# Kernel optimization log

Measured on AMD Instinct MI355X. Metric: run time of the kernel, lower is better.

Reference implementation:

```python
import jax, jax.numpy as jnp
import numpy as np

HID, H, HKV, D, INT, S, T = 2048, 16, 8, 128, 6144, 4096, 512
POS = 0          # absolute position of the first token in this prefill chunk
EPS = 1e-6
SCALE = 1.0 / D ** 0.5
REP = H // HKV


def setup_inputs() -> dict:
    key = jax.random.key(0)
    ks = jax.random.split(key, 12)
    w = lambda k, sh: jax.random.normal(k, sh, dtype=jnp.float32) * 0.02

    hidden_conv = jax.random.normal(ks[0], (1, HID, 1, T), dtype=jnp.float32)

    # RoPE tables for absolute positions POS..POS+T-1, HF half-rotation layout
    inv_freq = 1.0 / (10000.0 ** (jnp.arange(0, D, 2, dtype=jnp.float32) / D))
    pos = (POS + jnp.arange(T, dtype=jnp.float32))
    ang = pos[:, None] * inv_freq[None, :]                      # (T, D/2)
    emb = jnp.concatenate([ang, ang], axis=-1)                  # (T, D)
    cos = jnp.cos(emb)[None]                                    # (1, T, D)
    sin = jnp.sin(emb)[None]

    # one-hot write mask: column t has a 1 at row POS+t
    update_mask = jnp.zeros((S, T), jnp.float32).at[POS + jnp.arange(T), jnp.arange(T)].set(1.0)[None, None]
    # causal mask over the cache: slot s visible to token t iff s <= POS+t
    attn_mask = jnp.where(jnp.arange(S)[None, :] <= (POS + jnp.arange(T))[:, None], 0.0, -1e4).astype(jnp.float32)[None, None]

    k_cache = jnp.zeros((1, HKV, S, D), jnp.float32)
    v_cache = jnp.zeros((1, HKV, S, D), jnp.float32)

    return dict(
        hidden_conv=hidden_conv, cos=cos, sin=sin,
        update_mask=update_mask, attn_mask=attn_mask,
        k_cache=k_cache, v_cache=v_cache,
        wq=w(ks[1], (H * D, HID)), wk=w(ks[2], (HKV * D, HID)),
        wv=w(ks[3], (HKV * D, HID)), wo=w(ks[4], (HID, H * D)),
        ln1_w=jnp.ones((HID,), jnp.float32), ln2_w=jnp.ones((HID,), jnp.float32),
        qn_w=jnp.ones((D,), jnp.float32), kn_w=jnp.ones((D,), jnp.float32),
        w_gate_up=w(ks[5], (2 * INT, HID)), w_down=w(ks[6], (HID, INT)),
    )


def _rms(x, w):
    return x * jax.lax.rsqrt(jnp.mean(x * x, axis=-1, keepdims=True) + EPS) * w


def _rotate_half(x):
    x1, x2 = jnp.split(x, 2, axis=-1)
    return jnp.concatenate([-x2, x1], axis=-1)


def reference(hidden_conv, cos, sin, update_mask, attn_mask, k_cache, v_cache,
              wq, wk, wv, wo, ln1_w, ln2_w, qn_w, kn_w, w_gate_up, w_down):
    # (1, HID, 1, T) conv layout -> (1, T, HID)
    x = jnp.transpose(hidden_conv[:, :, 0, :], (0, 2, 1))

    h = _rms(x, ln1_w)
    # 1x1 conv == linear; channel order h*D+d matches view(1,H,D,T)
    q = jnp.einsum('btc,oc->bto', h, wq).reshape(1, T, H, D).transpose(0, 2, 1, 3)    # (1,H,T,D)
    k = jnp.einsum('btc,oc->bto', h, wk).reshape(1, T, HKV, D).transpose(0, 2, 1, 3)  # (1,HKV,T,D)
    v = jnp.einsum('btc,oc->bto', h, wv).reshape(1, T, HKV, D).transpose(0, 2, 1, 3)

    q = _rms(q, qn_w)
    k = _rms(k, kn_w)

    cos_b = cos[:, None]  # (1,1,T,D)
    sin_b = sin[:, None]
    q = q * cos_b + _rotate_half(q) * sin_b
    k = k * cos_b + _rotate_half(k) * sin_b

    # matmul-based KV cache write via one-hot mask (faithful to original)
    k_inc = jnp.matmul(update_mask, k)                 # (1,HKV,S,D)
    v_inc = jnp.matmul(update_mask, v)
    write_any = jnp.sum(update_mask, axis=-1, keepdims=True)  # (1,1,S,1)
    k_full = k_cache * (1.0 - write_any) + k_inc
    v_full = v_cache * (1.0 - write_any) + v_inc

    k_rep = jnp.repeat(k_full, REP, axis=1)            # (1,H,S,D)
    v_rep = jnp.repeat(v_full, REP, axis=1)

    scores = jnp.einsum('bhtd,bhsd->bhts', q, k_rep) * SCALE + attn_mask  # (1,H,T,S)
    attn = jax.nn.softmax(scores, axis=-1)
    out = jnp.einsum('bhts,bhsd->bhtd', attn, v_rep)   # (1,H,T,D)

    o_in = out.transpose(0, 2, 1, 3).reshape(1, T, H * D)
    attn_out = jnp.einsum('btc,oc->bto', o_in, wo)
    hidden = x + attn_out

    h2 = _rms(hidden, ln2_w)
    gate_up = jnp.einsum('btc,oc->bto', h2, w_gate_up)
    gate, up = jnp.split(gate_up, 2, axis=-1)
    mlp = jnp.einsum('bti,oi->bto', jax.nn.silu(gate) * up, w_down)
    hidden = hidden + mlp

    hidden_out = jnp.transpose(hidden, (0, 2, 1))[:, :, None, :]  # back to (1,HID,1,T)
    return hidden_out, k_full, v_full


if __name__ == '__main__':
    outs = reference(**setup_inputs())
    print([o.shape for o in outs])
```

## Files before the change

### kernel.cpp

```cpp
#include <hip/hip_runtime.h>
#include <hip/hip_bf16.h>
#include <hip/hip_fp16.h>

#define TT 512
#define HIDD 2048
#define NH 16
#define NKV 8
#define DD 128
#define INTR 6144
#define SEQ 4096
#define SCALE 0.08838834764831845f

typedef __attribute__((ext_vector_type(8))) short short8;
typedef __attribute__((ext_vector_type(4))) float floatx4;

static __device__ __forceinline__ unsigned short f2b(float f) {
  unsigned int u = __float_as_uint(f);
  u += 0x7fffu + ((u >> 16) & 1u);
  return (unsigned short)(u >> 16);
}

static __device__ __forceinline__ unsigned int f2b2(float a, float b) {
  __hip_bfloat162 h = __float22bfloat162_rn(make_float2(a, b));
  return *reinterpret_cast<unsigned int*>(&h);
}


static __device__ __forceinline__ void gld16(const void* g, void* l) {
  __builtin_amdgcn_global_load_lds(
      (const __attribute__((address_space(1))) unsigned int*)g,
      (__attribute__((address_space(3))) unsigned int*)l, 16, 0, 0);
}

template <int BM, bool B16>
static __device__ __forceinline__ void stage_tile(const unsigned short* __restrict__ A, int lda,
                                                  const void* __restrict__ B, int ldb, int k0,
                                                  unsigned char* buf, int wave, int lane) {
  {
    const int rpw = BM >> 2;
    const int rl = lane >> 2;
    const int c8 = (lane & 3) << 3;
#pragma unroll
    for (int i = 0; i < BM / 64; ++i) {
      const int rbase = wave * rpw + i * 16;
      gld16(A + (size_t)(rbase + rl) * lda + k0 + c8, buf + (size_t)rbase * 64);
    }
  }
  unsigned char* Bb = buf + BM * 64;
  if constexpr (B16) {
    const unsigned short* Bh = (const unsigned short*)B;
    const int rl = lane >> 2;
    const int c8 = (lane & 3) << 3;
#pragma unroll
    for (int i = 0; i < 2; ++i) {
      const int rbase = wave * 32 + i * 16;
      gld16(Bh + (size_t)(rbase + rl) * ldb + k0 + c8, Bb + (size_t)rbase * 64);
    }
  } else {
    const float* Bf = (const float*)B;
    const int rl = lane >> 3;
    const int sp = lane & 7;
#pragma unroll
    for (int i = 0; i < 4; ++i) {
      const int rbase = wave * 32 + i * 8;
      const int r = rbase + rl;
      gld16(Bf + (size_t)r * ldb + k0 + ((sp ^ (r & 7)) << 2), Bb + (size_t)rbase * 128);
    }
  }
}

template <int BM, bool B16>
static __device__ __forceinline__ void frags_from(const unsigned char* buf, int wr, int wc,
                                                  int lrow, int koff,
                                                  short8 (&af)[BM / 32], short8 (&bfr)[4]) {
  const unsigned short* Ab = (const unsigned short*)buf;
#pragma unroll
  for (int mi = 0; mi < BM / 32; ++mi)
    af[mi] = *reinterpret_cast<const short8*>(Ab + (size_t)(wr + mi * 16 + lrow) * 32 + koff);
  if constexpr (B16) {
    const unsigned short* Bb = (const unsigned short*)(buf + BM * 64);
#pragma unroll
    for (int ni = 0; ni < 4; ++ni)
      bfr[ni] = *reinterpret_cast<const short8*>(Bb + (size_t)(wc + ni * 16 + lrow) * 32 + koff);
  } else {
    const float* Bf = (const float*)(buf + BM * 64);
    const int s0 = koff >> 2;
#pragma unroll
    for (int ni = 0; ni < 4; ++ni) {
      const int r = wc + ni * 16 + lrow;
      const float4 x = *reinterpret_cast<const float4*>(Bf + (size_t)r * 32 + ((s0 ^ (r & 7)) << 2));
      const float4 y = *reinterpret_cast<const float4*>(Bf + (size_t)r * 32 + (((s0 + 1) ^ (r & 7)) << 2));
      union { short8 s; unsigned int u[4]; } pk;
      pk.u[0] = f2b2(x.x, x.y); pk.u[1] = f2b2(x.z, x.w);
      pk.u[2] = f2b2(y.x, y.y); pk.u[3] = f2b2(y.z, y.w);
      bfr[ni] = pk.s;
    }
  }
}

template <int BM, bool B16>
static __device__ __forceinline__ void gemm_core(const unsigned short* __restrict__ A, int lda,
                                                 const void* __restrict__ B, int ldb,
                                                 int kbeg, int kend, floatx4 (&acc)[BM / 32][4],
                                                 unsigned char* Ls) {
  constexpr int MI = BM / 32;
  constexpr int TILE = BM * 64 + (B16 ? 8192 : 16384);
  constexpr int NB = (BM / 64) + (B16 ? 2 : 4);
  const int tid = threadIdx.x;
  const int lane = tid & 63, wave = tid >> 6;
  const int wr = (wave >> 1) * (BM >> 1);
  const int wc = (wave & 1) << 6;
  const int lrow = lane & 15;
  const int koff = (lane >> 4) << 3;
  const int NT = (kend - kbeg) >> 5;
  stage_tile<BM, B16>(A, lda, B, ldb, kbeg,      Ls,        wave, lane);
  stage_tile<BM, B16>(A, lda, B, ldb, kbeg + 32, Ls + TILE, wave, lane);
  int p = 0;
  for (int t = 0; t < NT - 1; ++t) {
    if constexpr (NB == 6)      asm volatile("s_waitcnt vmcnt(6)" ::: "memory");
    else if constexpr (NB == 3) asm volatile("s_waitcnt vmcnt(3)" ::: "memory");
    else if constexpr (NB == 4) asm volatile("s_waitcnt vmcnt(4)" ::: "memory");
    else                        asm volatile("s_waitcnt vmcnt(5)" ::: "memory");
    __builtin_amdgcn_sched_barrier(0);
    __builtin_amdgcn_s_barrier();
    short8 af[MI], bfr[4];
    frags_from<BM, B16>(Ls + p * TILE, wr, wc, lrow, koff, af, bfr);
    asm volatile("s_waitcnt lgkmcnt(0)" ::: "memory");
    __builtin_amdgcn_sched_barrier(0);
    __builtin_amdgcn_s_barrier();
    if (t + 2 < NT)
      stage_tile<BM, B16>(A, lda, B, ldb, kbeg + (t + 2) * 32, Ls + p * TILE, wave, lane);
#pragma unroll
    for (int mi = 0; mi < MI; ++mi)
#pragma unroll
      for (int ni = 0; ni < 4; ++ni)
        acc[mi][ni] = __builtin_amdgcn_mfma_f32_16x16x32_bf16(af[mi], bfr[ni], acc[mi][ni], 0, 0, 0);
    p ^= 1;
  }
  asm volatile("s_waitcnt vmcnt(0)" ::: "memory");
  __builtin_amdgcn_sched_barrier(0);
  __builtin_amdgcn_s_barrier();
  {
    short8 af[MI], bfr[4];
    frags_from<BM, B16>(Ls + p * TILE, wr, wc, lrow, koff, af, bfr);
#pragma unroll
    for (int mi = 0; mi < MI; ++mi)
#pragma unroll
      for (int ni = 0; ni < 4; ++ni)
        acc[mi][ni] = __builtin_amdgcn_mfma_f32_16x16x32_bf16(af[mi], bfr[ni], acc[mi][ni], 0, 0, 0);
  }
}

#define EPI_VARS \
  const int lane = threadIdx.x & 63; \
  const int wave = threadIdx.x >> 6; \
  const int wc = (wave & 1) << 6;    \
  const int lrow = lane & 15;        \
  const int quad = lane >> 4;

#define ZERO_ACC(MI_) \
  floatx4 acc[MI_][4]; \
  _Pragma("unroll") for (int mi = 0; mi < MI_; ++mi) \
  _Pragma("unroll") for (int ni = 0; ni < 4; ++ni) { floatx4 z = {0.f, 0.f, 0.f, 0.f}; acc[mi][ni] = z; }

template <int S>
static __device__ __forceinline__ void swz(int b, int& mt, int& nt, int& s) {
  mt = (b >> 3) & 3;
  const int gid = ((b >> 5) << 3) | (b & 7);
  nt = gid / S;
  s = gid - nt * S;
}


__global__ __launch_bounds__(1024) void k_rms1(const float* __restrict__ conv,
                                               const float* __restrict__ w,
                                               float* __restrict__ xb,
                                               unsigned short* __restrict__ h1b) {
  const int t0 = blockIdx.x << 5;
  const int tid = threadIdx.x;
  const int j = tid & 31;
  const int g = tid >> 5;
  __shared__ float part[32][32];
  __shared__ float tile[32][33];
  __shared__ float rs[32];
  float ss = 0.f;
  for (int c0 = 0; c0 < HIDD; c0 += 32) {
    const float v = conv[(size_t)(c0 + g) * TT + t0 + j];
    ss += v * v;
  }
  part[g][j] = ss;
  __syncthreads();
  if (g == 0) {
    float tot = 0.f;
#pragma unroll
    for (int q = 0; q < 32; ++q) tot += part[q][j];
    rs[j] = rsqrtf(tot * (1.0f / HIDD) + 1e-6f);
  }
  __syncthreads();
  for (int c0 = 0; c0 < HIDD; c0 += 32) {
    tile[g][j] = conv[(size_t)(c0 + g) * TT + t0 + j];
    __syncthreads();
    const float v = tile[j][g];
    const float rv = rs[g];
    xb[(size_t)(t0 + g) * HIDD + c0 + j] = v;
    h1b[(size_t)(t0 + g) * HIDD + c0 + j] = f2b(v * rv * w[c0 + j]);
    __syncthreads();
  }
}

__global__ __launch_bounds__(256) void k_gemm_qkv(const unsigned short* __restrict__ h1b,
                                                  const float* __restrict__ wq,
                                                  const float* __restrict__ wk,
                                                  const float* __restrict__ wv,
                                                  float* __restrict__ Pq) {
  __shared__ __align__(16) unsigned char Ls[2 * (128 * 64 + 16384)];
  int mt, nt, s;
  swz<4>(blockIdx.x, mt, nt, s);
  const int m0 = mt << 7, n0 = nt << 7;
  const float* Bp;
  if (n0 < 2048)      Bp = wq + (size_t)n0 * HIDD;
  else if (n0 < 3072) Bp = wk + (size_t)(n0 - 2048) * HIDD;
  else                Bp = wv + (size_t)(n0 - 3072) * HIDD;
  ZERO_ACC(4)
  gemm_core<128, false>(h1b + (size_t)m0 * HIDD, HIDD, Bp, HIDD, s * 512, s * 512 + 512, acc, Ls);
  EPI_VARS
  const int wr = (wave >> 1) << 6;
  float* out = Pq + (size_t)s * (TT * 4096);
#pragma unroll
  for (int mi = 0; mi < 4; ++mi)
#pragma unroll
    for (int ni = 0; ni < 4; ++ni)
#pragma unroll
      for (int rr = 0; rr < 4; ++rr) {
        const int row = m0 + wr + mi * 16 + quad * 4 + rr;
        const int col = n0 + wc + ni * 16 + lrow;
        out[(size_t)row * 4096 + col] = acc[mi][ni][rr];
      }
}

__global__ __launch_bounds__(128) void k_rope(const float* __restrict__ Pq,
                                              const float* __restrict__ cosb,
                                              const float* __restrict__ sinb,
                                              const float* __restrict__ qnw,
                                              const float* __restrict__ knw,
                                              unsigned short* __restrict__ qb,
                                              unsigned short* __restrict__ kb,
                                              unsigned short* __restrict__ vtb,
                                              float* __restrict__ kout,
                                              float* __restrict__ vout) {
  const int u = blockIdx.x;
  const int t = blockIdx.y;
  const int d = threadIdx.x;
  __shared__ float red[2];
  __shared__ float sh[DD];
  int slot;
  if (u < NH)            slot = u * DD + d;
  else if (u < NH + NKV) slot = 2048 + (u - NH) * DD + d;
  else                   slot = 3072 + (u - NH - NKV) * DD + d;
  const size_t idx = (size_t)t * 4096 + slot;
  float val = Pq[idx] + Pq[idx + TT * 4096] + Pq[idx + 2 * TT * 4096] + Pq[idx + 3 * TT * 4096];
  if (u < NH + NKV) {
    float ss = val * val;
    const int lane = d & 63, wid = d >> 6;
#pragma unroll
    for (int o = 32; o; o >>= 1) ss += __shfl_xor(ss, o);
    if (!lane) red[wid] = ss;
    __syncthreads();
    const float r = rsqrtf((red[0] + red[1]) * (1.0f / DD) + 1e-6f);
    const float w = (u < NH) ? qnw[d] : knw[d];
    const float nv = val * r * w;
    sh[d] = nv;
    __syncthreads();
    const float partner = sh[d ^ 64];
    const float rh = (d < 64) ? -partner : partner;
    const float o = nv * cosb[(size_t)t * DD + d] + rh * sinb[(size_t)t * DD + d];
    if (u < NH) {
      qb[(size_t)u * TT * DD + (size_t)t * DD + d] = f2b(o);
    } else {
      const int kh = u - NH;
      kout[(size_t)kh * SEQ * DD + (size_t)t * DD + d] = o;
      kb[(size_t)kh * TT * DD + (size_t)t * DD + d] = f2b(o);
    }
  } else {
    const int vh = u - NH - NKV;
    vout[(size_t)vh * SEQ * DD + (size_t)t * DD + d] = val;
    vtb[(size_t)vh * DD * TT + (size_t)d * TT + t] = f2b(val);
  }
}

__global__ __launch_bounds__(256) void k_tail(const float* __restrict__ kc,
                                              const float* __restrict__ vc,
                                              float* __restrict__ ko,
                                              float* __restrict__ vo) {
  const int i = blockIdx.x * 256 + threadIdx.x;
  const int e = i << 2;
  const int s = (e >> 7) & (SEQ - 1);
  if (s >= TT) {
    reinterpret_cast<float4*>(ko)[i] = reinterpret_cast<const float4*>(kc)[i];
    reinterpret_cast<float4*>(vo)[i] = reinterpret_cast<const float4*>(vc)[i];
  }
}

__global__ __launch_bounds__(256) void k_scores(const unsigned short* __restrict__ qb,
                                                const unsigned short* __restrict__ kb,
                                                float* __restrict__ sc) {
  __shared__ __align__(16) unsigned char Ls[2 * (64 * 64 + 8192)];
  const int m0 = blockIdx.x << 6, n0 = blockIdx.y << 7, h = blockIdx.z;
  ZERO_ACC(2)
  gemm_core<64, true>(qb + (size_t)h * TT * DD + (size_t)m0 * DD, DD,
                      kb + (size_t)(h >> 1) * TT * DD + (size_t)n0 * DD, DD, 0, DD, acc, Ls);
  EPI_VARS
  const int wr = (wave >> 1) << 5;
  float* out = sc + (size_t)h * TT * TT;
#pragma unroll
  for (int mi = 0; mi < 2; ++mi)
#pragma unroll
    for (int ni = 0; ni < 4; ++ni)
#pragma unroll
      for (int rr = 0; rr < 4; ++rr) {
        const int t = m0 + wr + mi * 16 + quad * 4 + rr;
        const int s = n0 + wc + ni * 16 + lrow;
        float v = acc[mi][ni][rr] * SCALE;
        if (s > t) v += -10000.0f;
        out[(size_t)t * TT + s] = v;
      }
}

__global__ __launch_bounds__(256) void k_softmax(const float* __restrict__ sc,
                                                 unsigned short* __restrict__ Pb) {
  const int h = blockIdx.x >> 9, t = blockIdx.x & 511;
  const int tid = threadIdx.x;
  const float* row = sc + ((size_t)h * TT + t) * TT;
  float v0 = row[tid], v1 = row[tid + 256];
  __shared__ float red[4];
  const int lane = tid & 63, wid = tid >> 6;
  float m = fmaxf(v0, v1);
#pragma unroll
  for (int o = 32; o; o >>= 1) m = fmaxf(m, __shfl_xor(m, o));
  if (!lane) red[wid] = m;
  __syncthreads();
  m = fmaxf(fmaxf(red[0], red[1]), fmaxf(red[2], red[3]));
  const float e0 = __expf(v0 - m), e1 = __expf(v1 - m);
  float s = e0 + e1;
  __syncthreads();
#pragma unroll
  for (int o = 32; o; o >>= 1) s += __shfl_xor(s, o);
  if (!lane) red[wid] = s;
  __syncthreads();
  const float inv = 1.0f / (red[0] + red[1] + red[2] + red[3]);
  unsigned short* orow = Pb + ((size_t)h * TT + t) * TT;
  orow[tid] = f2b(e0 * inv);
  orow[tid + 256] = f2b(e1 * inv);
}

__global__ __launch_bounds__(256) void k_pv(const unsigned short* __restrict__ Pb,
                                            const unsigned short* __restrict__ vtb,
                                            float* __restrict__ Ppv) {
  __shared__ __align__(16) unsigned char Ls[2 * (64 * 64 + 8192)];
  const int m0 = blockIdx.x << 6, h = blockIdx.y, s = blockIdx.z;
  ZERO_ACC(2)
  gemm_core<64, true>(Pb + (size_t)h * TT * TT + (size_t)m0 * TT, TT,
                      vtb + (size_t)(h >> 1) * DD * TT, TT, s * 128, s * 128 + 128, acc, Ls);
  EPI_VARS
  const int wr = (wave >> 1) << 5;
  float* out = Ppv + (size_t)s * (TT * HIDD);
#pragma unroll
  for (int mi = 0; mi < 2; ++mi)
#pragma unroll
    for (int ni = 0; ni < 4; ++ni)
#pragma unroll
      for (int rr = 0; rr < 4; ++rr) {
        const int row = m0 + wr + mi * 16 + quad * 4 + rr;
        const int col = wc + ni * 16 + lrow;
        out[(size_t)row * HIDD + h * DD + col] = acc[mi][ni][rr];
      }
}

__global__ __launch_bounds__(256) void k_red_pv(const float* __restrict__ Ppv,
                                                unsigned short* __restrict__ o_inb) {
  const int i = blockIdx.x * 256 + threadIdx.x;
  const float4* p = reinterpret_cast<const float4*>(Ppv);
  float4 a = p[i];
  const float4 b = p[i + 262144], c = p[i + 524288], d = p[i + 786432];
  a.x += b.x + c.x + d.x; a.y += b.y + c.y + d.y;
  a.z += b.z + c.z + d.z; a.w += b.w + c.w + d.w;
  uint2 o;
  o.x = f2b2(a.x, a.y);
  o.y = f2b2(a.z, a.w);
  *reinterpret_cast<uint2*>(o_inb + (size_t)i * 4) = o;
}

__global__ __launch_bounds__(256) void k_gemm_o(const unsigned short* __restrict__ o_inb,
                                                const float* __restrict__ wo,
                                                float* __restrict__ Po) {
  __shared__ __align__(16) unsigned char Ls[2 * (128 * 64 + 16384)];
  int mt, nt, s;
  swz<8>(blockIdx.x, mt, nt, s);
  const int m0 = mt << 7, n0 = nt << 7;
  ZERO_ACC(4)
  gemm_core<128, false>(o_inb + (size_t)m0 * HIDD, HIDD, wo + (size_t)n0 * HIDD, HIDD,
                        s * 256, s * 256 + 256, acc, Ls);
  EPI_VARS
  const int wr = (wave >> 1) << 6;
  float* out = Po + (size_t)s * (TT * HIDD);
#pragma unroll
  for (int mi = 0; mi < 4; ++mi)
#pragma unroll
    for (int ni = 0; ni < 4; ++ni)
#pragma unroll
      for (int rr = 0; rr < 4; ++rr) {
        const int row = m0 + wr + mi * 16 + quad * 4 + rr;
        const int col = n0 + wc + ni * 16 + lrow;
        out[(size_t)row * HIDD + col] = acc[mi][ni][rr];
      }
}

__global__ __launch_bounds__(256) void k_rms2(const float* __restrict__ xb,
                                              const float* __restrict__ Po,
                                              const float* __restrict__ w,
                                              float* __restrict__ hidden,
                                              unsigned short* __restrict__ h2b) {
  const int t = blockIdx.x;
  const int tid = threadIdx.x;
  float2 v[4];
  float ss = 0.f;
#pragma unroll
  for (int i = 0; i < 4; ++i) {
    const int c = (tid << 1) + (i << 9);
    const size_t idx = (size_t)t * HIDD + c;
    float2 a = *reinterpret_cast<const float2*>(xb + idx);
#pragma unroll
    for (int sp = 0; sp < 8; ++sp) {
      const float2 b = *reinterpret_cast<const float2*>(Po + idx + (size_t)sp * (TT * HIDD));
      a.x += b.x; a.y += b.y;
    }
    v[i] = a;
    ss += a.x * a.x + a.y * a.y;
  }
  __shared__ float red[4];
  const int lane = tid & 63, wid = tid >> 6;
#pragma unroll
  for (int o = 32; o; o >>= 1) ss += __shfl_xor(ss, o);
  if (!lane) red[wid] = ss;
  __syncthreads();
  const float tot = red[0] + red[1] + red[2] + red[3];
  const float r = rsqrtf(tot * (1.0f / HIDD) + 1e-6f);
#pragma unroll
  for (int i = 0; i < 4; ++i) {
    const int c = (tid << 1) + (i << 9);
    const size_t idx = (size_t)t * HIDD + c;
    *reinterpret_cast<float2*>(hidden + idx) = v[i];
    const float2 wv2 = *reinterpret_cast<const float2*>(w + c);
    *reinterpret_cast<unsigned int*>(h2b + idx) = f2b2(v[i].x * r * wv2.x, v[i].y * r * wv2.y);
  }
}

__global__ __launch_bounds__(256) void k_gemm_gu(const unsigned short* __restrict__ h2b,
                                                 const float* __restrict__ wgu,
                                                 __half* __restrict__ guh) {
  __shared__ __align__(16) unsigned char Ls[2 * (128 * 64 + 16384)];
  int mt, nt, s;
  swz<2>(blockIdx.x, mt, nt, s);
  const int m0 = mt << 7, n0 = nt << 7;
  ZERO_ACC(4)
  gemm_core<128, false>(h2b + (size_t)m0 * HIDD, HIDD, wgu + (size_t)n0 * HIDD, HIDD,
                        s * 1024, s * 1024 + 1024, acc, Ls);
  EPI_VARS
  const int wr = (wave >> 1) << 6;
  __half* out = guh + (size_t)s * (TT * 2 * INTR);
#pragma unroll
  for (int mi = 0; mi < 4; ++mi)
#pragma unroll
    for (int ni = 0; ni < 4; ++ni)
#pragma unroll
      for (int rr = 0; rr < 4; ++rr) {
        const int row = m0 + wr + mi * 16 + quad * 4 + rr;
        const int col = n0 + wc + ni * 16 + lrow;
        out[(size_t)row * (2 * INTR) + col] = __float2half(acc[mi][ni][rr]);
      }
}

__global__ __launch_bounds__(256) void k_silu(const __half* __restrict__ guh,
                                              unsigned short* __restrict__ actb) {
  const int j0 = (blockIdx.x * 256 + threadIdx.x) << 1;
  const int t = blockIdx.y;
  const size_t base = (size_t)t * (2 * INTR) + j0;
  const size_t off = (size_t)TT * (2 * INTR);
  const float2 g0 = __half22float2(*reinterpret_cast<const __half2*>(guh + base));
  const float2 g1 = __half22float2(*reinterpret_cast<const __half2*>(guh + off + base));
  const float2 u0 = __half22float2(*reinterpret_cast<const __half2*>(guh + base + INTR));
  const float2 u1 = __half22float2(*reinterpret_cast<const __half2*>(guh + off + base + INTR));
  const float gx = g0.x + g1.x, gy = g0.y + g1.y;
  const float ux = u0.x + u1.x, uy = u0.y + u1.y;
  const float a0 = gx / (1.f + __expf(-gx)) * ux;
  const float a1 = gy / (1.f + __expf(-gy)) * uy;
  *reinterpret_cast<unsigned int*>(actb + (size_t)t * INTR + j0) = f2b2(a0, a1);
}

__global__ __launch_bounds__(256) void k_gemm_down(const unsigned short* __restrict__ actb,
                                                   const float* __restrict__ wdn,
                                                   float* __restrict__ Pdn) {
  __shared__ __align__(16) unsigned char Ls[2 * (128 * 64 + 16384)];
  int mt, nt, s;
  swz<8>(blockIdx.x, mt, nt, s);
  const int m0 = mt << 7, n0 = nt << 7;
  ZERO_ACC(4)
  gemm_core<128, false>(actb + (size_t)m0 * INTR, INTR, wdn + (size_t)n0 * INTR, INTR,
                        s * 768, s * 768 + 768, acc, Ls);
  EPI_VARS
  const int wr = (wave >> 1) << 6;
  float* out = Pdn + (size_t)s * (TT * HIDD);
#pragma unroll
  for (int mi = 0; mi < 4; ++mi)
#pragma unroll
    for (int ni = 0; ni < 4; ++ni)
#pragma unroll
      for (int rr = 0; rr < 4; ++rr) {
        const int row = m0 + wr + mi * 16 + quad * 4 + rr;
        const int col = n0 + wc + ni * 16 + lrow;
        out[(size_t)row * HIDD + col] = acc[mi][ni][rr];
      }
}

__global__ __launch_bounds__(256) void k_final(const float* __restrict__ hidden,
                                               const float* __restrict__ Pdn,
                                               float* __restrict__ out0) {
  __shared__ float tile[32][33];
  const int c0 = blockIdx.x << 5, t0 = blockIdx.y << 5;
  const int tx = threadIdx.x & 31, ty0 = (threadIdx.x >> 5) << 2;
#pragma unroll
  for (int i = 0; i < 4; ++i) {
    const int t = t0 + ty0 + i;
    const size_t idx = (size_t)t * HIDD + c0 + tx;
    float a = hidden[idx];
#pragma unroll
    for (int sp = 0; sp < 8; ++sp) a += Pdn[idx + (size_t)sp * (TT * HIDD)];
    tile[ty0 + i][tx] = a;
  }
  __syncthreads();
#pragma unroll
  for (int i = 0; i < 4; ++i)
    out0[(size_t)(c0 + ty0 + i) * TT + t0 + tx] = tile[tx][ty0 + i];
}

extern "C" void kernel_launch(void* const* d_in, const int* in_sizes, int n_in,
                              void* d_out, int out_size, void* d_ws, size_t ws_size,
                              hipStream_t stream) {
  const float* conv   = (const float*)d_in[0];
  const float* cosb   = (const float*)d_in[1];
  const float* sinb   = (const float*)d_in[2];
  const float* kcache = (const float*)d_in[5];
  const float* vcache = (const float*)d_in[6];
  const float* wq  = (const float*)d_in[7];
  const float* wk  = (const float*)d_in[8];
  const float* wv  = (const float*)d_in[9];
  const float* wo  = (const float*)d_in[10];
  const float* ln1 = (const float*)d_in[11];
  const float* ln2 = (const float*)d_in[12];
  const float* qnw = (const float*)d_in[13];
  const float* knw = (const float*)d_in[14];
  const float* wgu = (const float*)d_in[15];
  const float* wdn = (const float*)d_in[16];

  float* ws = (float*)d_ws;
  float* xb = ws + 0;
  unsigned short* h1b  = (unsigned short*)(ws + 1048576);
  unsigned short* o_inb = h1b;
  unsigned short* h2b  = (unsigned short*)(ws + 1572864);
  float* hidden = ws + 2097152;
  unsigned short* qb  = (unsigned short*)(ws + 3145728);
  unsigned short* kb  = qb + 1048576;
  unsigned short* vtb = kb + 524288;
  unsigned short* actb = (unsigned short*)(ws + 4194304);
  float* R   = ws + 5767168;
  float* Pq  = R;
  unsigned short* Pb = (unsigned short*)R;
  float* sc  = R + 2097152;
  float* Ppv = R + 2097152;
  float* Po  = R;
  __half* guh = (__half*)R;
  float* Pdn = R;

  float* out0 = (float*)d_out;
  float* kout = out0 + 1048576;
  float* vout = kout + 4194304;

  k_rms1<<<16, 1024, 0, stream>>>(conv, ln1, xb, h1b);
  k_gemm_qkv<<<512, 256, 0, stream>>>(h1b, wq, wk, wv, Pq);
  k_rope<<<dim3(NH + 2 * NKV, TT), 128, 0, stream>>>(Pq, cosb, sinb, qnw, knw, qb, kb, vtb, kout, vout);
  k_tail<<<4096, 256, 0, stream>>>(kcache, vcache, kout, vout);
  k_scores<<<dim3(8, 4, NH), 256, 0, stream>>>(qb, kb, sc);
  k_softmax<<<NH * TT, 256, 0, stream>>>(sc, Pb);
  k_pv<<<dim3(8, NH, 4), 256, 0, stream>>>(Pb, vtb, Ppv);
  k_red_pv<<<1024, 256, 0, stream>>>(Ppv, o_inb);
  k_gemm_o<<<512, 256, 0, stream>>>(o_inb, wo, Po);
  k_rms2<<<TT, 256, 0, stream>>>(xb, Po, ln2, hidden, h2b);
  k_gemm_gu<<<768, 256, 0, stream>>>(h2b, wgu, guh);
  k_silu<<<dim3(12, TT), 256, 0, stream>>>(guh, actb);
  k_gemm_down<<<512, 256, 0, stream>>>(actb, wdn, Pdn);
  k_final<<<dim3(HIDD / 32, TT / 32), 256, 0, stream>>>(hidden, Pdn, out0);
}
```

Measured before the change: 465.4 us.

## Use triple-buffered LDS ring in GEMM core to drop one barrier per k-step

Switches the shared GEMM main loop from a double buffer to a three-slot LDS ring. The next tile is now staged into a third slot while the current slot is read, so each iteration needs only one barrier instead of two plus an lgkmcnt wait. This trades 50% more LDS per block, which may reduce occupancy in the 128-row GEMMs (72 KB per block), for less synchronisation stall.

```diff
diff --git a/kernel.cpp b/kernel.cpp
--- a/kernel.cpp
+++ b/kernel.cpp
@@ -113,41 +113,31 @@
   const int lrow = lane & 15;
   const int koff = (lane >> 4) << 3;
   const int NT = (kend - kbeg) >> 5;
-  stage_tile<BM, B16>(A, lda, B, ldb, kbeg,      Ls,        wave, lane);
-  stage_tile<BM, B16>(A, lda, B, ldb, kbeg + 32, Ls + TILE, wave, lane);
-  int p = 0;
-  for (int t = 0; t < NT - 1; ++t) {
-    if constexpr (NB == 6)      asm volatile("s_waitcnt vmcnt(6)" ::: "memory");
-    else if constexpr (NB == 3) asm volatile("s_waitcnt vmcnt(3)" ::: "memory");
-    else if constexpr (NB == 4) asm volatile("s_waitcnt vmcnt(4)" ::: "memory");
-    else                        asm volatile("s_waitcnt vmcnt(5)" ::: "memory");
+  unsigned char* P0 = Ls;
+  unsigned char* P1 = Ls + TILE;
+  unsigned char* P2 = Ls + 2 * TILE;
+  stage_tile<BM, B16>(A, lda, B, ldb, kbeg,      P0, wave, lane);
+  stage_tile<BM, B16>(A, lda, B, ldb, kbeg + 32, P1, wave, lane);
+  for (int t = 0; t < NT; ++t) {
+    if (t + 1 < NT) {
+      if constexpr (NB == 6)      asm volatile("s_waitcnt vmcnt(6)" ::: "memory");
+      else if constexpr (NB == 4) asm volatile("s_waitcnt vmcnt(4)" ::: "memory");
+      else                        asm volatile("s_waitcnt vmcnt(3)" ::: "memory");
+    } else {
+      asm volatile("s_waitcnt vmcnt(0)" ::: "memory");
+    }
+    __builtin_amdgcn_s_barrier();
     __builtin_amdgcn_sched_barrier(0);
-    __builtin_amdgcn_s_barrier();
+    if (t + 2 < NT)
+      stage_tile<BM, B16>(A, lda, B, ldb, kbeg + (t + 2) * 32, P2, wave, lane);
     short8 af[MI], bfr[4];
-    frags_from<BM, B16>(Ls + p * TILE, wr, wc, lrow, koff, af, bfr);
-    asm volatile("s_waitcnt lgkmcnt(0)" ::: "memory");
-    __builtin_amdgcn_sched_barrier(0);
-    __builtin_amdgcn_s_barrier();
-    if (t + 2 < NT)
-      stage_tile<BM, B16>(A, lda, B, ldb, kbeg + (t + 2) * 32, Ls + p * TILE, wave, lane);
+    frags_from<BM, B16>(P0, wr, wc, lrow, koff, af, bfr);
 #pragma unroll
     for (int mi = 0; mi < MI; ++mi)
 #pragma unroll
       for (int ni = 0; ni < 4; ++ni)
         acc[mi][ni] = __builtin_amdgcn_mfma_f32_16x16x32_bf16(af[mi], bfr[ni], acc[mi][ni], 0, 0, 0);
-    p ^= 1;
-  }
-  asm volatile("s_waitcnt vmcnt(0)" ::: "memory");
-  __builtin_amdgcn_sched_barrier(0);
-  __builtin_amdgcn_s_barrier();
-  {
-    short8 af[MI], bfr[4];
-    frags_from<BM, B16>(Ls + p * TILE, wr, wc, lrow, koff, af, bfr);
-#pragma unroll
-    for (int mi = 0; mi < MI; ++mi)
-#pragma unroll
-      for (int ni = 0; ni < 4; ++ni)
-        acc[mi][ni] = __builtin_amdgcn_mfma_f32_16x16x32_bf16(af[mi], bfr[ni], acc[mi][ni], 0, 0, 0);
+    unsigned char* tmp = P0; P0 = P1; P1 = P2; P2 = tmp;
   }
 }
 
@@ -213,7 +203,7 @@
                                                   const float* __restrict__ wk,
                                                   const float* __restrict__ wv,
                                                   float* __restrict__ Pq) {
-  __shared__ __align__(16) unsigned char Ls[2 * (128 * 64 + 16384)];
+  __shared__ __align__(16) unsigned char Ls[3 * (128 * 64 + 16384)];
   int mt, nt, s;
   swz<4>(blockIdx.x, mt, nt, s);
   const int m0 = mt << 7, n0 = nt << 7;
@@ -304,7 +294,7 @@
 __global__ __launch_bounds__(256) void k_scores(const unsigned short* __restrict__ qb,
                                                 const unsigned short* __restrict__ kb,
                                                 float* __restrict__ sc) {
-  __shared__ __align__(16) unsigned char Ls[2 * (64 * 64 + 8192)];
+  __shared__ __align__(16) unsigned char Ls[3 * (64 * 64 + 8192)];
   const int m0 = blockIdx.x << 6, n0 = blockIdx.y << 7, h = blockIdx.z;
   ZERO_ACC(2)
   gemm_core<64, true>(qb + (size_t)h * TT * DD + (size_t)m0 * DD, DD,
@@ -356,7 +346,7 @@
 __global__ __launch_bounds__(256) void k_pv(const unsigned short* __restrict__ Pb,
                                             const unsigned short* __restrict__ vtb,
                                             float* __restrict__ Ppv) {
-  __shared__ __align__(16) unsigned char Ls[2 * (64 * 64 + 8192)];
+  __shared__ __align__(16) unsigned char Ls[3 * (64 * 64 + 8192)];
   const int m0 = blockIdx.x << 6, h = blockIdx.y, s = blockIdx.z;
   ZERO_ACC(2)
   gemm_core<64, true>(Pb + (size_t)h * TT * TT + (size_t)m0 * TT, TT,
@@ -393,7 +383,7 @@
 __global__ __launch_bounds__(256) void k_gemm_o(const unsigned short* __restrict__ o_inb,
                                                 const float* __restrict__ wo,
                                                 float* __restrict__ Po) {
-  __shared__ __align__(16) unsigned char Ls[2 * (128 * 64 + 16384)];
+  __shared__ __align__(16) unsigned char Ls[3 * (128 * 64 + 16384)];
   int mt, nt, s;
   swz<8>(blockIdx.x, mt, nt, s);
   const int m0 = mt << 7, n0 = nt << 7;
@@ -458,7 +448,7 @@
 __global__ __launch_bounds__(256) void k_gemm_gu(const unsigned short* __restrict__ h2b,
                                                  const float* __restrict__ wgu,
                                                  __half* __restrict__ guh) {
-  __shared__ __align__(16) unsigned char Ls[2 * (128 * 64 + 16384)];
+  __shared__ __align__(16) unsigned char Ls[3 * (128 * 64 + 16384)];
   int mt, nt, s;
   swz<2>(blockIdx.x, mt, nt, s);
   const int m0 = mt << 7, n0 = nt << 7;
@@ -500,7 +490,7 @@
 __global__ __launch_bounds__(256) void k_gemm_down(const unsigned short* __restrict__ actb,
                                                    const float* __restrict__ wdn,
                                                    float* __restrict__ Pdn) {
-  __shared__ __align__(16) unsigned char Ls[2 * (128 * 64 + 16384)];
+  __shared__ __align__(16) unsigned char Ls[3 * (128 * 64 + 16384)];
   int mt, nt, s;
   swz<8>(blockIdx.x, mt, nt, s);
   const int m0 = mt << 7, n0 = nt << 7;
```

Measured after the change: 486.4 us. 4.5% more time.
